# Kernel tuning notes

Hardware: AMD Instinct MI355X
Metric: run time of the kernel (lower is better)

Reference implementation:

```python
import jax, jax.numpy as jnp
import numpy as np

B, D, T_STEPS = 256, 512, 256


def setup_inputs() -> dict:
    key = jax.random.key(0)
    k1, k2 = jax.random.split(key)
    # Scale K like flax lecun_normal init (std = 1/sqrt(fan_in)) so rollout stays stable.
    z0 = jax.random.normal(k1, (B, D), dtype=jnp.float32)
    K = jax.random.normal(k2, (D, D), dtype=jnp.float32) / np.sqrt(D)
    return {"z0": z0, "K": K, "T": T_STEPS}


def reference(z0, K, T):
    # z_{t+1} = z_t @ K  (flax Linear with use_bias=False: y = x @ kernel)
    def step(z, _):
        z_next = z @ K  # [B, D] @ [D, D] -> [B, D]
        return z_next, z_next

    _, preds = jax.lax.scan(step, z0, xs=None, length=T)  # [T, B, D]
    return jnp.transpose(preds, (1, 0, 2))  # [B, T, D]
```

## Files before the change

kernel.cpp:

```cpp
#include <hip/hip_runtime.h>


typedef unsigned short u16;
typedef unsigned int u32;
typedef __bf16 bf16x8 __attribute__((ext_vector_type(8)));
typedef float f32x4 __attribute__((ext_vector_type(4)));
typedef u16 u16x4 __attribute__((ext_vector_type(4)));
typedef u16 u16x8 __attribute__((ext_vector_type(8)));

#define MAT 262144
#define SLOT 1048576
#define WSLOT 131072

__device__ __forceinline__ u16 f2b(float f) {
  u32 x = __float_as_uint(f);
  return (u16)((x + 0x7fffu + ((x >> 16) & 1u)) >> 16);
}
__device__ __forceinline__ float b2f(u16 u) { return __uint_as_float(((u32)u) << 16); }

__device__ __forceinline__ size_t pidx(int r, int k) {
  return (size_t)(((r >> 4) * 16 + (k >> 5)) * 512 + ((k >> 3) & 3) * 128 + (r & 15) * 8 + (k & 7));
}

__device__ __forceinline__ void gll16(const void* g, void* l) {
  __builtin_amdgcn_global_load_lds((__attribute__((address_space(1))) void*)(void*)g,
                                   (__attribute__((address_space(3))) void*)l, 16, 0, 0);
}

__global__ __launch_bounds__(256) void prep_kernel(const float* __restrict__ Kc,
                                                   const float* __restrict__ z0,
                                                   u16* __restrict__ P,
                                                   u16* __restrict__ Uh,
                                                   u16* __restrict__ Ul) {
  int tid = threadIdx.x, b = blockIdx.x;
  if (b < 64) {
    int r0 = (b >> 3) * 64, c0b = (b & 7) * 64;
#pragma unroll
    for (int q = 0; q < 2; ++q) {
      int g = q * 256 + tid;
      int r = r0 + (g >> 3), c0 = c0b + (g & 7) * 8;
      float4 v0 = *(const float4*)(Kc + (size_t)r * 512 + c0);
      float4 v1 = *(const float4*)(Kc + (size_t)r * 512 + c0 + 4);
      float v[8] = {v0.x, v0.y, v0.z, v0.w, v1.x, v1.y, v1.z, v1.w};
      u16x8 h8, l8v;
#pragma unroll
      for (int j = 0; j < 8; ++j) {
        u16 h = f2b(v[j]);
        h8[j] = h;
        l8v[j] = f2b(v[j] - b2f(h));
        size_t ib = pidx(c0 + j, r);
        P[2 * MAT + ib] = h;
        P[3 * MAT + ib] = l8v[j];
      }
      size_t ia = pidx(r, c0);
      *(u16x8*)(P + ia) = h8;
      *(u16x8*)(P + MAT + ia) = l8v;
    }
  } else {
    int idb = b - 64;
#pragma unroll
    for (int q = 0; q < 4; ++q) {
      int g = (idb * 4 + q) * 256 + tid;
      int r = g >> 6, c0 = (g & 63) * 8;
      float4 v0 = *(const float4*)(z0 + (size_t)r * 512 + c0);
      float4 v1 = *(const float4*)(z0 + (size_t)r * 512 + c0 + 4);
      float v[8] = {v0.x, v0.y, v0.z, v0.w, v1.x, v1.y, v1.z, v1.w};
      u16x8 h8, l8v;
#pragma unroll
      for (int j = 0; j < 8; ++j) {
        u16 h = f2b(v[j]);
        h8[j] = h;
        l8v[j] = f2b(v[j] - b2f(h));
      }
      size_t ia = pidx(r, c0);
      *(u16x8*)(Uh + ia) = h8;
      *(u16x8*)(Ul + ia) = l8v;
    }
  }
}

__global__ __launch_bounds__(256, 2) void gemm_stage(
    const u16* __restrict__ fA, long fAstr,
    u16* __restrict__ fC, long fCstr,
    const u16* __restrict__ Bh, int nfull, int rowmask, int tlomask,
    const u16* __restrict__ UA, u16* __restrict__ UC) {
  __shared__ u16 Bs[32768];
  int z = blockIdx.z, y = blockIdx.y;
  const u16 *Ah, *Al;
  u16 *Ch, *Clo, *CTh, *CTl;
  int m0;
  bool full = (y < 8 * nfull);
  bool wrow, wtlo;
  if (full) {
    Ah = fA + (size_t)z * fAstr;
    Al = Ah + MAT;
    Ch = fC + (size_t)z * fCstr;
    Clo = Ch + MAT;
    CTh = Ch + 2 * MAT;
    CTl = Ch + 3 * MAT;
    m0 = y * 64;
    wrow = (rowmask >> z) & 1;
    wtlo = (tlomask >> z) & 1;
  } else {
    int yy = y - 8 * nfull;
    int u = yy >> 2;
    Ah = UA + (size_t)u * WSLOT;
    Al = Ah + 16 * (size_t)WSLOT;
    Ch = UC + (size_t)u * WSLOT;
    Clo = Ch + 16 * (size_t)WSLOT;
    CTh = CTl = nullptr;
    m0 = (yy & 3) * 64;
    wrow = true;
    wtlo = false;
  }
  const u16* Bl = Bh + MAT;
  int tid = threadIdx.x;
  int n0 = blockIdx.x * 32;
  int wv = tid >> 6, lane = tid & 63;
  int mrow = lane & 15, quad = lane >> 4;
  int l8 = lane * 8;
  int nchunk0 = n0 >> 4;
  const u16* ph = Bh + (size_t)nchunk0 * 16 * 512;
  const u16* pl = Bl + (size_t)nchunk0 * 16 * 512;
#pragma unroll
  for (int i = 0; i < 8; ++i) {
    int ch = wv * 8 + i;
    gll16(ph + (size_t)ch * 512 + l8, Bs + ch * 512);
    gll16(pl + (size_t)ch * 512 + l8, Bs + 16384 + ch * 512);
  }
  __syncthreads();
  int mc = (m0 >> 4) + wv;
  f32x4 acc[2] = {};
#pragma unroll 4
  for (int kt = 0; kt < 16; ++kt) {
    size_t co = (size_t)(mc * 16 + kt) * 512 + l8;
    bf16x8 ah = *(const bf16x8*)(Ah + co);
    bf16x8 al = *(const bf16x8*)(Al + co);
#pragma unroll
    for (int nt = 0; nt < 2; ++nt) {
      bf16x8 bh = *(const bf16x8*)(Bs + (nt * 16 + kt) * 512 + l8);
      bf16x8 bl = *(const bf16x8*)(Bs + 16384 + (nt * 16 + kt) * 512 + l8);
      acc[nt] = __builtin_amdgcn_mfma_f32_16x16x32_bf16(ah, bh, acc[nt], 0, 0, 0);
      acc[nt] = __builtin_amdgcn_mfma_f32_16x16x32_bf16(al, bh, acc[nt], 0, 0, 0);
      acc[nt] = __builtin_amdgcn_mfma_f32_16x16x32_bf16(ah, bl, acc[nt], 0, 0, 0);
    }
  }
  int mbase = m0 + wv * 16 + quad * 4;
#pragma unroll
  for (int nt = 0; nt < 2; ++nt) {
    int n = n0 + nt * 16 + mrow;
    u16x4 h4, l4;
#pragma unroll
    for (int r = 0; r < 4; ++r) {
      float v = acc[nt][r];
      u16 h = f2b(v);
      h4[r] = h;
      l4[r] = f2b(v - b2f(h));
    }
    if (wrow) {
#pragma unroll
      for (int r = 0; r < 4; ++r) {
        size_t ia = pidx(mbase + r, n);
        Ch[ia] = h4[r];
        Clo[ia] = l4[r];
      }
    }
    if (full) {
      size_t ib = pidx(n, mbase);
      *(u16x4*)(CTh + ib) = h4;
      if (wtlo) *(u16x4*)(CTl + ib) = l4;
    }
  }
}

__global__ __launch_bounds__(256, 2) void gemm_out(const u16* __restrict__ Wb,
                                                   const u16* __restrict__ PT0,
                                                   float* __restrict__ out) {
  __shared__ u16 Bs[32768];
  int z = blockIdx.z;
  const u16* A = Wb + (size_t)(z >> 4) * WSLOT;
  const u16* Bt = PT0 + (size_t)(z & 15) * SLOT;
  int tid = threadIdx.x;
  int n0 = blockIdx.x * 64;
  int wv = tid >> 6, lane = tid & 63;
  int mrow = lane & 15, quad = lane >> 4;
  int l8 = lane * 8;
  const u16* pb = Bt + (size_t)(n0 >> 4) * 16 * 512;
#pragma unroll
  for (int i = 0; i < 16; ++i) {
    int ch = wv * 16 + i;
    gll16(pb + (size_t)ch * 512 + l8, Bs + ch * 512);
  }
  __syncthreads();
  int mc0 = wv * 4;
  f32x4 acc[4][4] = {};
#pragma unroll 4
  for (int kt = 0; kt < 16; ++kt) {
    bf16x8 a[4], b[4];
#pragma unroll
    for (int mt = 0; mt < 4; ++mt)
      a[mt] = *(const bf16x8*)(A + (size_t)((mc0 + mt) * 16 + kt) * 512 + l8);
#pragma unroll
    for (int nt = 0; nt < 4; ++nt)
      b[nt] = *(const bf16x8*)(Bs + (nt * 16 + kt) * 512 + l8);
#pragma unroll
    for (int mt = 0; mt < 4; ++mt)
#pragma unroll
      for (int nt = 0; nt < 4; ++nt)
        acc[mt][nt] = __builtin_amdgcn_mfma_f32_16x16x32_bf16(a[mt], b[nt], acc[mt][nt], 0, 0, 0);
  }
#pragma unroll
  for (int mt = 0; mt < 4; ++mt)
#pragma unroll
    for (int nt = 0; nt < 4; ++nt) {
      int gb = wv * 64 + mt * 16 + quad * 4;
      int gd = n0 + nt * 16 + mrow;
#pragma unroll
      for (int r = 0; r < 4; ++r)
        out[((size_t)(gb + r) * 256 + z) * 512 + gd] = acc[mt][nt][r];
    }
}

extern "C" void kernel_launch(void* const* d_in, const int* in_sizes, int n_in,
                              void* d_out, int out_size, void* d_ws, size_t ws_size,
                              hipStream_t stream) {
  const float* z0 = (const float*)d_in[0];
  const float* Kc = (const float*)d_in[1];
  float* out = (float*)d_out;
  u16* Uh = (u16*)d_ws;
  u16* Ul = Uh + 16 * (size_t)WSLOT;
  u16* P = Ul + 16 * (size_t)WSLOT;
  auto S = [&](int s) { return P + (size_t)s * SLOT; };
  dim3 blk(256);

  prep_kernel<<<80, blk, 0, stream>>>(Kc, z0, P, Uh, Ul);
  gemm_stage<<<dim3(16, 8, 1), blk, 0, stream>>>(S(0), 0, S(1), 0, S(0) + 2 * MAT, 1, 0x1, 0x1, nullptr, nullptr);
  gemm_stage<<<dim3(16, 8, 2), blk, 0, stream>>>(S(0), SLOT, S(2), SLOT, S(1) + 2 * MAT, 1, 0x3, 0x2, nullptr, nullptr);
  gemm_stage<<<dim3(16, 8, 4), blk, 0, stream>>>(S(0), SLOT, S(4), SLOT, S(3) + 2 * MAT, 1, 0xF, 0x8, nullptr, nullptr);
  gemm_stage<<<dim3(16, 8, 8), blk, 0, stream>>>(S(0), SLOT, S(8), SLOT, S(7) + 2 * MAT, 1, 0x80, 0x80, nullptr, nullptr);
  gemm_stage<<<dim3(16, 12, 1), blk, 0, stream>>>(S(15), 0, S(16), 0, S(15) + 2 * MAT, 1, 0x1, 0x1, Uh, Uh + 1 * (size_t)WSLOT);
  gemm_stage<<<dim3(16, 16, 1), blk, 0, stream>>>(S(16), 0, S(17), 0, S(16) + 2 * MAT, 1, 0x1, 0x1, Uh, Uh + 2 * (size_t)WSLOT);
  gemm_stage<<<dim3(16, 24, 1), blk, 0, stream>>>(S(17), 0, S(18), 0, S(17) + 2 * MAT, 1, 0x0, 0x1, Uh, Uh + 4 * (size_t)WSLOT);
  gemm_stage<<<dim3(16, 32, 1), blk, 0, stream>>>(S(18), 0, S(18), 0, S(18) + 2 * MAT, 0, 0x0, 0x0, Uh, Uh + 8 * (size_t)WSLOT);
  gemm_out<<<dim3(8, 1, 256), blk, 0, stream>>>(Uh, P + 2 * MAT, out);
}
```

Before: 248.9 us.

## Fuse all stage launches into one cooperative persistent kernel with grid syncs

The prep, eight GEMM stages and the output GEMM become device functions called from a single cooperative kernel. Blocks loop over job indices and separate stages with grid.sync() instead of kernel boundaries. This removes the launch gaps and tail drains between the nine dependent launches. The cost is grid-wide barrier overhead, a per-stage parameter table read from device memory, and a grid capped at 512 blocks that may serialize the large output phase.

```diff
diff --git a/kernel.cpp b/kernel.cpp
--- a/kernel.cpp
+++ b/kernel.cpp
@@ -1,5 +1,8 @@
 #include <hip/hip_runtime.h>
-
+#include <hip/hip_cooperative_groups.h>
+
+
+namespace cg = cooperative_groups;
 
 typedef unsigned short u16;
 typedef unsigned int u32;
@@ -27,12 +30,9 @@
                                    (__attribute__((address_space(3))) void*)l, 16, 0, 0);
 }
 
-__global__ __launch_bounds__(256) void prep_kernel(const float* __restrict__ Kc,
-                                                   const float* __restrict__ z0,
-                                                   u16* __restrict__ P,
-                                                   u16* __restrict__ Uh,
-                                                   u16* __restrict__ Ul) {
-  int tid = threadIdx.x, b = blockIdx.x;
+__device__ __forceinline__ void prep_job(int b, int tid, const float* __restrict__ Kc,
+                                         const float* __restrict__ z0, u16* __restrict__ P,
+                                         u16* __restrict__ Uh, u16* __restrict__ Ul) {
   if (b < 64) {
     int r0 = (b >> 3) * 64, c0b = (b & 7) * 64;
 #pragma unroll
@@ -79,17 +79,15 @@
   }
 }
 
-__global__ __launch_bounds__(256, 2) void gemm_stage(
-    const u16* __restrict__ fA, long fAstr,
-    u16* __restrict__ fC, long fCstr,
-    const u16* __restrict__ Bh, int nfull, int rowmask, int tlomask,
+__device__ __forceinline__ void stage_job(
+    u16* Bs, int tid, int x, int y, int z,
+    const u16* __restrict__ fA, long fAstr, u16* __restrict__ fC, long fCstr,
+    const u16* __restrict__ Bh, int nfullv, int rowmask, int tlomask,
     const u16* __restrict__ UA, u16* __restrict__ UC) {
-  __shared__ u16 Bs[32768];
-  int z = blockIdx.z, y = blockIdx.y;
   const u16 *Ah, *Al;
   u16 *Ch, *Clo, *CTh, *CTl;
   int m0;
-  bool full = (y < 8 * nfull);
+  bool full = (y < 8 * nfullv);
   bool wrow, wtlo;
   if (full) {
     Ah = fA + (size_t)z * fAstr;
@@ -102,7 +100,7 @@
     wrow = (rowmask >> z) & 1;
     wtlo = (tlomask >> z) & 1;
   } else {
-    int yy = y - 8 * nfull;
+    int yy = y - 8 * nfullv;
     int u = yy >> 2;
     Ah = UA + (size_t)u * WSLOT;
     Al = Ah + 16 * (size_t)WSLOT;
@@ -114,8 +112,7 @@
     wtlo = false;
   }
   const u16* Bl = Bh + MAT;
-  int tid = threadIdx.x;
-  int n0 = blockIdx.x * 32;
+  int n0 = x * 32;
   int wv = tid >> 6, lane = tid & 63;
   int mrow = lane & 15, quad = lane >> 4;
   int l8 = lane * 8;
@@ -173,15 +170,13 @@
   }
 }
 
-__global__ __launch_bounds__(256, 2) void gemm_out(const u16* __restrict__ Wb,
-                                                   const u16* __restrict__ PT0,
-                                                   float* __restrict__ out) {
-  __shared__ u16 Bs[32768];
-  int z = blockIdx.z;
+__device__ __forceinline__ void out_job(u16* Bs, int tid, int x, int z,
+                                        const u16* __restrict__ Wb,
+                                        const u16* __restrict__ PT0,
+                                        float* __restrict__ out) {
   const u16* A = Wb + (size_t)(z >> 4) * WSLOT;
   const u16* Bt = PT0 + (size_t)(z & 15) * SLOT;
-  int tid = threadIdx.x;
-  int n0 = blockIdx.x * 64;
+  int n0 = x * 64;
   int wv = tid >> 6, lane = tid & 63;
   int mrow = lane & 15, quad = lane >> 4;
   int l8 = lane * 8;
@@ -221,26 +216,74 @@
     }
 }
 
+struct SP {
+  int asl, astrf, csl, cstrf, bsl, nfull, rm, tm, uoff, ny;
+  int nz;
+};
+__device__ const SP g_sp[8] = {
+    {0, 0, 1, 0, 0, 1, 0x1, 0x1, 0, 8, 1},
+    {0, 1, 2, 1, 1, 1, 0x3, 0x2, 0, 8, 2},
+    {0, 1, 4, 1, 3, 1, 0xF, 0x8, 0, 8, 4},
+    {0, 1, 8, 1, 7, 1, 0x80, 0x80, 0, 8, 8},
+    {15, 0, 16, 0, 15, 1, 0x1, 0x1, 1, 12, 1},
+    {16, 0, 17, 0, 16, 1, 0x1, 0x1, 2, 16, 1},
+    {17, 0, 18, 0, 17, 1, 0x0, 0x1, 4, 24, 1},
+    {18, 0, 18, 0, 18, 0, 0x0, 0x0, 8, 32, 1},
+};
+
+__global__ __launch_bounds__(256, 2) void fused(const float* Kc, const float* z0,
+                                                u16* P, u16* Uh, u16* Ul, float* out) {
+  __shared__ u16 Bs[32768];
+  cg::grid_group grid = cg::this_grid();
+  int tid = threadIdx.x;
+  int nb = gridDim.x, bid = blockIdx.x;
+
+  for (int b = bid; b < 80; b += nb) prep_job(b, tid, Kc, z0, P, Uh, Ul);
+  grid.sync();
+
+#pragma unroll 1
+  for (int s = 0; s < 8; ++s) {
+    SP p = g_sp[s];
+    const u16* fA = P + (size_t)p.asl * SLOT;
+    u16* fC = P + (size_t)p.csl * SLOT;
+    const u16* Bh = P + (size_t)p.bsl * SLOT + 2 * MAT;
+    long astr = p.astrf ? (long)SLOT : 0;
+    long cstr = p.cstrf ? (long)SLOT : 0;
+    u16* UC = Uh + (size_t)p.uoff * WSLOT;
+    int njobs = 16 * p.ny * p.nz;
+    for (int j = bid; j < njobs; j += nb) {
+      int x = j & 15, q = j >> 4;
+      int y = q % p.ny, z = q / p.ny;
+      stage_job(Bs, tid, x, y, z, fA, astr, fC, cstr, Bh, p.nfull, p.rm, p.tm, Uh, UC);
+      __syncthreads();
+    }
+    grid.sync();
+  }
+
+  for (int j = bid; j < 2048; j += nb) {
+    out_job(Bs, tid, j & 7, j >> 3, Uh, P + 2 * MAT, out);
+    __syncthreads();
+  }
+}
+
 extern "C" void kernel_launch(void* const* d_in, const int* in_sizes, int n_in,
                               void* d_out, int out_size, void* d_ws, size_t ws_size,
                               hipStream_t stream) {
+  const float* Kc = (const float*)d_in[1];
   const float* z0 = (const float*)d_in[0];
-  const float* Kc = (const float*)d_in[1];
   float* out = (float*)d_out;
   u16* Uh = (u16*)d_ws;
   u16* Ul = Uh + 16 * (size_t)WSLOT;
   u16* P = Ul + 16 * (size_t)WSLOT;
-  auto S = [&](int s) { return P + (size_t)s * SLOT; };
-  dim3 blk(256);
-
-  prep_kernel<<<80, blk, 0, stream>>>(Kc, z0, P, Uh, Ul);
-  gemm_stage<<<dim3(16, 8, 1), blk, 0, stream>>>(S(0), 0, S(1), 0, S(0) + 2 * MAT, 1, 0x1, 0x1, nullptr, nullptr);
-  gemm_stage<<<dim3(16, 8, 2), blk, 0, stream>>>(S(0), SLOT, S(2), SLOT, S(1) + 2 * MAT, 1, 0x3, 0x2, nullptr, nullptr);
-  gemm_stage<<<dim3(16, 8, 4), blk, 0, stream>>>(S(0), SLOT, S(4), SLOT, S(3) + 2 * MAT, 1, 0xF, 0x8, nullptr, nullptr);
-  gemm_stage<<<dim3(16, 8, 8), blk, 0, stream>>>(S(0), SLOT, S(8), SLOT, S(7) + 2 * MAT, 1, 0x80, 0x80, nullptr, nullptr);
-  gemm_stage<<<dim3(16, 12, 1), blk, 0, stream>>>(S(15), 0, S(16), 0, S(15) + 2 * MAT, 1, 0x1, 0x1, Uh, Uh + 1 * (size_t)WSLOT);
-  gemm_stage<<<dim3(16, 16, 1), blk, 0, stream>>>(S(16), 0, S(17), 0, S(16) + 2 * MAT, 1, 0x1, 0x1, Uh, Uh + 2 * (size_t)WSLOT);
-  gemm_stage<<<dim3(16, 24, 1), blk, 0, stream>>>(S(17), 0, S(18), 0, S(17) + 2 * MAT, 1, 0x0, 0x1, Uh, Uh + 4 * (size_t)WSLOT);
-  gemm_stage<<<dim3(16, 32, 1), blk, 0, stream>>>(S(18), 0, S(18), 0, S(18) + 2 * MAT, 0, 0x0, 0x0, Uh, Uh + 8 * (size_t)WSLOT);
-  gemm_out<<<dim3(8, 1, 256), blk, 0, stream>>>(Uh, P + 2 * MAT, out);
-}
+
+  static int nblk = 0;
+  if (!nblk) {
+    int per = 0;
+    if (hipOccupancyMaxActiveBlocksPerMultiprocessor(&per, (const void*)fused, 256, 0) != hipSuccess || per <= 0)
+      per = 2;
+    int cap = per * 256;
+    nblk = cap < 512 ? cap : 512;
+  }
+  void* args[] = {(void*)&Kc, (void*)&z0, (void*)&P, (void*)&Uh, (void*)&Ul, (void*)&out};
+  hipLaunchCooperativeKernel((const void*)fused, dim3(nblk), dim3(256), args, 0, stream);
+}
```

Measured after the change: 581.1 us. 133% more time.

## Fuse all stages into one persistent kernel with an atomic job queue and dependency counters

Applied to the files above, without the earlier changes.

Replaces the prep launch, eight staged GEMM launches and the output GEMM launch with a single persistent kernel. Blocks pull job indices from a global atomic counter. Each job range waits on a per-stage completion counter before it runs. This removes launch gaps and lets slices of the output GEMM run alongside later doubling stages instead of waiting for the whole chain. The cost is spin-waiting, extra atomics and fences, and a control block placed inside the workspace, which must not alias live data.

```diff
diff --git a/kernel.cpp b/kernel.cpp
--- a/kernel.cpp
+++ b/kernel.cpp
@@ -11,6 +11,7 @@
 #define MAT 262144
 #define SLOT 1048576
 #define WSLOT 131072
+#define NJOBS 5392
 
 __device__ __forceinline__ u16 f2b(float f) {
   u32 x = __float_as_uint(f);
@@ -27,12 +28,9 @@
                                    (__attribute__((address_space(3))) void*)l, 16, 0, 0);
 }
 
-__global__ __launch_bounds__(256) void prep_kernel(const float* __restrict__ Kc,
-                                                   const float* __restrict__ z0,
-                                                   u16* __restrict__ P,
-                                                   u16* __restrict__ Uh,
-                                                   u16* __restrict__ Ul) {
-  int tid = threadIdx.x, b = blockIdx.x;
+__device__ void prep_job(int b, int tid, const float* __restrict__ Kc,
+                         const float* __restrict__ z0, u16* __restrict__ P,
+                         u16* __restrict__ Uh, u16* __restrict__ Ul) {
   if (b < 64) {
     int r0 = (b >> 3) * 64, c0b = (b & 7) * 64;
 #pragma unroll
@@ -79,34 +77,45 @@
   }
 }
 
-__global__ __launch_bounds__(256, 2) void gemm_stage(
-    const u16* __restrict__ fA, long fAstr,
-    u16* __restrict__ fC, long fCstr,
-    const u16* __restrict__ Bh, int nfull, int rowmask, int tlomask,
-    const u16* __restrict__ UA, u16* __restrict__ UC) {
-  __shared__ u16 Bs[32768];
-  int z = blockIdx.z, y = blockIdx.y;
+struct LP { int asl, astrf, csl, cstrf, bsl, nfull, rm, tm, uoff, ny; };
+__device__ const LP g_lp[8] = {
+    {0, 0, 1, 0, 0, 1, 0x1, 0x1, 0, 8},
+    {0, 1, 2, 1, 1, 1, 0x3, 0x2, 0, 8},
+    {0, 1, 4, 1, 3, 1, 0xF, 0x8, 0, 8},
+    {0, 1, 8, 1, 7, 1, 0x80, 0x80, 0, 8},
+    {15, 0, 16, 0, 15, 1, 0x1, 0x1, 1, 12},
+    {16, 0, 17, 0, 16, 1, 0x1, 0x1, 2, 16},
+    {17, 0, 18, 0, 17, 1, 0x0, 0x1, 4, 24},
+    {18, 0, 18, 0, 18, 0, 0x0, 0x0, 8, 32},
+};
+
+__device__ void stage_job(u16* Bs, int tid, int x, int y, int z, const LP& p,
+                          u16* __restrict__ P, u16* __restrict__ Uh,
+                          u16* __restrict__ Ul) {
+  const u16* fA = P + (size_t)p.asl * SLOT;
+  u16* fC = P + (size_t)p.csl * SLOT;
+  const u16* Bh = P + (size_t)p.bsl * SLOT + 2 * MAT;
   const u16 *Ah, *Al;
   u16 *Ch, *Clo, *CTh, *CTl;
   int m0;
-  bool full = (y < 8 * nfull);
+  bool full = (y < 8 * p.nfull);
   bool wrow, wtlo;
   if (full) {
-    Ah = fA + (size_t)z * fAstr;
+    Ah = fA + (size_t)z * (p.astrf ? SLOT : 0);
     Al = Ah + MAT;
-    Ch = fC + (size_t)z * fCstr;
+    Ch = fC + (size_t)z * (p.cstrf ? SLOT : 0);
     Clo = Ch + MAT;
     CTh = Ch + 2 * MAT;
     CTl = Ch + 3 * MAT;
     m0 = y * 64;
-    wrow = (rowmask >> z) & 1;
-    wtlo = (tlomask >> z) & 1;
+    wrow = (p.rm >> z) & 1;
+    wtlo = (p.tm >> z) & 1;
   } else {
-    int yy = y - 8 * nfull;
+    int yy = y - 8 * p.nfull;
     int u = yy >> 2;
-    Ah = UA + (size_t)u * WSLOT;
+    Ah = Uh + (size_t)u * WSLOT;
     Al = Ah + 16 * (size_t)WSLOT;
-    Ch = UC + (size_t)u * WSLOT;
+    Ch = Uh + (size_t)(p.uoff + u) * WSLOT;
     Clo = Ch + 16 * (size_t)WSLOT;
     CTh = CTl = nullptr;
     m0 = (yy & 3) * 64;
@@ -114,8 +123,7 @@
     wtlo = false;
   }
   const u16* Bl = Bh + MAT;
-  int tid = threadIdx.x;
-  int n0 = blockIdx.x * 32;
+  int n0 = x * 32;
   int wv = tid >> 6, lane = tid & 63;
   int mrow = lane & 15, quad = lane >> 4;
   int l8 = lane * 8;
@@ -173,15 +181,12 @@
   }
 }
 
-__global__ __launch_bounds__(256, 2) void gemm_out(const u16* __restrict__ Wb,
-                                                   const u16* __restrict__ PT0,
-                                                   float* __restrict__ out) {
-  __shared__ u16 Bs[32768];
-  int z = blockIdx.z;
-  const u16* A = Wb + (size_t)(z >> 4) * WSLOT;
-  const u16* Bt = PT0 + (size_t)(z & 15) * SLOT;
-  int tid = threadIdx.x;
-  int n0 = blockIdx.x * 64;
+__device__ void out_job(u16* Bs, int tid, int x, int zo,
+                        const u16* __restrict__ Ub, const u16* __restrict__ PT0,
+                        float* __restrict__ out) {
+  const u16* A = Ub + (size_t)(zo >> 4) * WSLOT;
+  const u16* Bt = PT0 + (size_t)(zo & 15) * SLOT;
+  int n0 = x * 64;
   int wv = tid >> 6, lane = tid & 63;
   int mrow = lane & 15, quad = lane >> 4;
   int l8 = lane * 8;
@@ -217,8 +222,75 @@
       int gd = n0 + nt * 16 + mrow;
 #pragma unroll
       for (int r = 0; r < 4; ++r)
-        out[((size_t)(gb + r) * 256 + z) * 512 + gd] = acc[mt][nt][r];
-    }
+        out[((size_t)(gb + r) * 256 + zo) * 512 + gd] = acc[mt][nt][r];
+    }
+}
+
+struct RG { int start, kind, prm, dep, need, sig; };
+__device__ const RG g_rg[18] = {
+    {0,    0, 0,  -1, 0,    0},
+    {80,   1, 0,   0, 80,   1},
+    {208,  2, 0,   0, 80,  -1},
+    {216,  1, 1,   1, 128,  2},
+    {472,  2, 1,   1, 128, -1},
+    {480,  1, 2,   2, 256,  3},
+    {992,  2, 2,   2, 256, -1},
+    {1008, 1, 3,   3, 512,  4},
+    {2032, 2, 4,   3, 512, -1},
+    {2064, 1, 4,   4, 1024, 5},
+    {2256, 2, 8,   4, 1024,-1},
+    {2320, 1, 5,   5, 192,  6},
+    {2576, 2, 16,  5, 192, -1},
+    {2704, 1, 6,   6, 256,  7},
+    {3088, 2, 32,  6, 256, -1},
+    {3344, 1, 7,   7, 384,  8},
+    {3856, 2, 64,  7, 384, -1},
+    {4368, 2, 128, 8, 512, -1},
+};
+
+__global__ __launch_bounds__(256, 2) void mega(const float* Kc, const float* z0,
+                                               u16* P, u16* Uh, u16* Ul,
+                                               float* out, u32* ctrl) {
+  __shared__ u16 Bs[32768];
+  __shared__ int sh_t;
+  int tid = threadIdx.x;
+  for (;;) {
+    __syncthreads();
+    if (tid == 0) sh_t = (int)atomicAdd(ctrl, 1u);
+    __syncthreads();
+    int t = sh_t;
+    if (t >= NJOBS) return;
+    int ri = 0;
+#pragma unroll
+    for (int i = 1; i < 18; ++i)
+      if (t >= g_rg[i].start) ri = i;
+    RG rg = g_rg[ri];
+    if (rg.dep >= 0) {
+      if (tid == 0) {
+        u32* c = ctrl + 1 + rg.dep;
+        while ((int)__hip_atomic_load(c, __ATOMIC_RELAXED, __HIP_MEMORY_SCOPE_AGENT) < rg.need)
+          __builtin_amdgcn_s_sleep(8);
+        __threadfence();
+      }
+      __syncthreads();
+    }
+    int e = t - rg.start;
+    if (rg.kind == 0) {
+      prep_job(e, tid, Kc, z0, P, Uh, Ul);
+    } else if (rg.kind == 1) {
+      LP p = g_lp[rg.prm];
+      int x = e & 15, q = e >> 4;
+      stage_job(Bs, tid, x, q % p.ny, q / p.ny, p, P, Uh, Ul);
+    } else {
+      out_job(Bs, tid, e & 7, rg.prm + (e >> 3), Uh, P + 2 * MAT, out);
+    }
+    __syncthreads();
+    if (rg.sig >= 0 && tid == 0) {
+      __threadfence();
+      __hip_atomic_fetch_add(ctrl + 1 + rg.sig, 1u, __ATOMIC_RELAXED,
+                             __HIP_MEMORY_SCOPE_AGENT);
+    }
+  }
 }
 
 extern "C" void kernel_launch(void* const* d_in, const int* in_sizes, int n_in,
@@ -230,17 +302,8 @@
   u16* Uh = (u16*)d_ws;
   u16* Ul = Uh + 16 * (size_t)WSLOT;
   u16* P = Ul + 16 * (size_t)WSLOT;
-  auto S = [&](int s) { return P + (size_t)s * SLOT; };
-  dim3 blk(256);
-
-  prep_kernel<<<80, blk, 0, stream>>>(Kc, z0, P, Uh, Ul);
-  gemm_stage<<<dim3(16, 8, 1), blk, 0, stream>>>(S(0), 0, S(1), 0, S(0) + 2 * MAT, 1, 0x1, 0x1, nullptr, nullptr);
-  gemm_stage<<<dim3(16, 8, 2), blk, 0, stream>>>(S(0), SLOT, S(2), SLOT, S(1) + 2 * MAT, 1, 0x3, 0x2, nullptr, nullptr);
-  gemm_stage<<<dim3(16, 8, 4), blk, 0, stream>>>(S(0), SLOT, S(4), SLOT, S(3) + 2 * MAT, 1, 0xF, 0x8, nullptr, nullptr);
-  gemm_stage<<<dim3(16, 8, 8), blk, 0, stream>>>(S(0), SLOT, S(8), SLOT, S(7) + 2 * MAT, 1, 0x80, 0x80, nullptr, nullptr);
-  gemm_stage<<<dim3(16, 12, 1), blk, 0, stream>>>(S(15), 0, S(16), 0, S(15) + 2 * MAT, 1, 0x1, 0x1, Uh, Uh + 1 * (size_t)WSLOT);
-  gemm_stage<<<dim3(16, 16, 1), blk, 0, stream>>>(S(16), 0, S(17), 0, S(16) + 2 * MAT, 1, 0x1, 0x1, Uh, Uh + 2 * (size_t)WSLOT);
-  gemm_stage<<<dim3(16, 24, 1), blk, 0, stream>>>(S(17), 0, S(18), 0, S(17) + 2 * MAT, 1, 0x0, 0x1, Uh, Uh + 4 * (size_t)WSLOT);
-  gemm_stage<<<dim3(16, 32, 1), blk, 0, stream>>>(S(18), 0, S(18), 0, S(18) + 2 * MAT, 0, 0x0, 0x0, Uh, Uh + 8 * (size_t)WSLOT);
-  gemm_out<<<dim3(8, 1, 256), blk, 0, stream>>>(Uh, P + 2 * MAT, out);
-}
+  u32* ctrl = (u32*)(P + 8 * (size_t)SLOT);
+
+  hipMemsetAsync(ctrl, 0, 64, stream);
+  mega<<<dim3(512), dim3(256), 0, stream>>>(Kc, z0, P, Uh, Ul, out, ctrl);
+}
```

Result: slower. 776.3 us (+211.9%).
